# Kernel optimization log

Hardware: AMD Instinct MI355X
Metric: run time of the kernel (lower is better)

## Reference

```python
import jax, jax.numpy as jnp
import numpy as np

B, T, D = 1, 2048, 2048
H, KVH, G, HD = 32, 8, 4, 64  # n_heads, n_kv_heads, n_groups, head_dim


def _rope_angles(t, hd):
    # standard RoPE angle table: [T, hd//2]
    inv_freq = 1.0 / (10000.0 ** (jnp.arange(0, hd, 2, dtype=jnp.float32) / hd))
    return jnp.arange(t, dtype=jnp.float32)[:, None] * inv_freq[None, :]


def setup_inputs() -> dict:
    key = jax.random.key(0)
    k1, k2, k3, k4, k5 = jax.random.split(key, 5)
    scale = 0.02
    return {
        "x": jax.random.normal(k1, (B, T, D), dtype=jnp.float32),
        "freqs": _rope_angles(T, HD),                                  # [T, HD//2]
        "wq": jax.random.normal(k2, (D, H * HD), dtype=jnp.float32) * scale,
        "wk": jax.random.normal(k3, (D, KVH * HD), dtype=jnp.float32) * scale,
        "wv": jax.random.normal(k4, (D, KVH * HD), dtype=jnp.float32) * scale,
        "wo": jax.random.normal(k5, (H * HD, D), dtype=jnp.float32) * scale,
    }


def _apply_rope(t, cos, sin):
    # t: [B, T, nh, HD]; cos/sin: [T, HD//2] -> broadcast [1, T, 1, HD//2]
    t1, t2 = t[..., ::2], t[..., 1::2]
    c = cos[None, :, None, :]
    s = sin[None, :, None, :]
    out_even = t1 * c - t2 * s
    out_odd = t1 * s + t2 * c
    return jnp.stack([out_even, out_odd], axis=-1).reshape(t.shape)


def reference(x, freqs, wq, wk, wv, wo):
    b, t, _ = x.shape
    q = (x @ wq).reshape(b, t, H, HD)
    k = (x @ wk).reshape(b, t, KVH, HD)
    v = (x @ wv).reshape(b, t, KVH, HD)

    cos, sin = jnp.cos(freqs), jnp.sin(freqs)
    q = _apply_rope(q, cos, sin)
    k = _apply_rope(k, cos, sin)

    # GQA: repeat_interleave along head dim (kv head h -> query heads h*G..h*G+G-1)
    k = jnp.repeat(k, G, axis=2)  # [b, t, H, HD]
    v = jnp.repeat(v, G, axis=2)

    scale = 1.0 / jnp.sqrt(jnp.asarray(HD, dtype=x.dtype))
    scores = jnp.einsum("bthd,bshd->bhts", q, k) * scale  # [b, H, t, t]
    causal = jnp.tril(jnp.ones((t, t), dtype=bool))
    scores = jnp.where(causal[None, None], scores, jnp.asarray(-jnp.inf, dtype=scores.dtype))
    attn = jax.nn.softmax(scores, axis=-1)

    out = jnp.einsum("bhts,bshd->bthd", attn, v).reshape(b, t, H * HD)
    return out @ wo
```

## Files before the change

kernel.cpp:

```cpp
#include <hip/hip_runtime.h>
#include <cstdint>
#include <cstddef>

#define T_SEQ 2048
#define D_MODEL 2048
#define NH 32
#define NKVH 8
#define HDIM 64

typedef _Float16 f16;
typedef __attribute__((ext_vector_type(8))) _Float16 half8;
typedef __attribute__((ext_vector_type(4))) _Float16 half4;
typedef __attribute__((ext_vector_type(4))) float floatx4;

#define QSCALE 0.1803368801111204f

#if __has_builtin(__builtin_amdgcn_exp2f)
#define EXP2F(x) __builtin_amdgcn_exp2f(x)
#else
#define EXP2F(x) exp2f(x)
#endif


__device__ __forceinline__ void gload_lds16(const void* g, void* l) {
  __builtin_amdgcn_global_load_lds(
      (const __attribute__((address_space(1))) void*)g,
      (__attribute__((address_space(3))) void*)l,
      16, 0, 0);
}

__global__ __launch_bounds__(256) void cvt_f16_kernel(const float* __restrict__ in,
                                                      f16* __restrict__ out, int n4) {
  int id = blockIdx.x * 256 + threadIdx.x;
  if (id >= n4) return;
  int t = id >> 9;
  int d0 = (id & 511) * 4;
  float4 v = ((const float4*)in)[id];
  half4 o;
  o[0] = (f16)v.x; o[1] = (f16)v.y; o[2] = (f16)v.z; o[3] = (f16)v.w;
  int bm = t >> 7, mtb = (t & 127) >> 4, l15 = t & 15;
  int kt = d0 >> 6, s = (d0 & 63) >> 5, quad = (d0 & 31) >> 3, j = d0 & 7;
  size_t off = ((size_t)bm * 32 + kt) * 8192 + mtb * 1024 + s * 512 + (quad * 16 + l15) * 8 + j;
  *(half4*)&out[off] = o;
}

__global__ __launch_bounds__(256) void transpose_wqkv_kernel(const float* __restrict__ wq,
                                                             const float* __restrict__ wk,
                                                             const float* __restrict__ wv,
                                                             f16* __restrict__ out) {
  __shared__ f16 tile[64 * 65];
  int tid = threadIdx.x;
  int bx = blockIdx.x, kt = blockIdx.y;
  const float* in;
  int N, outN0, inCol0;
  if (bx < 32)      { in = wq; N = 2048; outN0 = 0;    inCol0 = bx * 64; }
  else if (bx < 40) { in = wk; N = 512;  outN0 = 2048; inCol0 = (bx - 32) * 64; }
  else              { in = wv; N = 512;  outN0 = 2560; inCol0 = (bx - 40) * 64; }
  int k0 = kt * 64;
#pragma unroll
  for (int i = 0; i < 16; i++) {
    int idx = i * 256 + tid;
    int kk = idx >> 6, nn = idx & 63;
    tile[nn * 65 + kk] = (f16)in[(size_t)(k0 + kk) * N + inCol0 + nn];
  }
  __syncthreads();
#pragma unroll
  for (int i = 0; i < 2; i++) {
    int idx = i * 256 + tid;
    int dd = idx >> 3, c = idx & 7;
    half8 v8 = *(const half8*)&tile[dd * 65 + c * 8];
    int ng = outN0 + inCol0 + dd;
    int bn = ng >> 7, ntb = (ng & 127) >> 4, l15 = ng & 15;
    int s = c >> 2, quad = c & 3;
    *(half8*)&out[((size_t)bn * 32 + kt) * 8192 + ntb * 1024 + s * 512 + (quad * 16 + l15) * 8] = v8;
  }
}

__global__ __launch_bounds__(256) void transpose_w_kernel(const float* __restrict__ in,
                                                          f16* __restrict__ out,
                                                          int N, int outN0) {
  __shared__ f16 tile[64 * 65];
  int tid = threadIdx.x;
  int inCol0 = blockIdx.x * 64, kt = blockIdx.y;
  int k0 = kt * 64;
#pragma unroll
  for (int i = 0; i < 16; i++) {
    int idx = i * 256 + tid;
    int kk = idx >> 6, nn = idx & 63;
    tile[nn * 65 + kk] = (f16)in[(size_t)(k0 + kk) * N + inCol0 + nn];
  }
  __syncthreads();
#pragma unroll
  for (int i = 0; i < 2; i++) {
    int idx = i * 256 + tid;
    int dd = idx >> 3, c = idx & 7;
    half8 v8 = *(const half8*)&tile[dd * 65 + c * 8];
    int ng = outN0 + inCol0 + dd;
    int bn = ng >> 7, ntb = (ng & 127) >> 4, l15 = ng & 15;
    int s = c >> 2, quad = c & 3;
    *(half8*)&out[((size_t)bn * 32 + kt) * 8192 + ntb * 1024 + s * 512 + (quad * 16 + l15) * 8] = v8;
  }
}

template <typename OutT>
__global__ __launch_bounds__(256) void gemm_f16_kernel(const f16* __restrict__ A,
                                                       const f16* __restrict__ BT,
                                                       OutT* __restrict__ C,
                                                       int M, int N, int K) {
  __shared__ alignas(16) f16 As[2][8192];
  __shared__ alignas(16) f16 Bs[2][8192];
  int tid = threadIdx.x;
  int wave = tid >> 6, lane = tid & 63;
  int ln15 = lane & 15, quad = lane >> 4;
  int wr = wave >> 1, wc = wave & 1;
  int bm = blockIdx.y, bn = blockIdx.x;
  int ktiles = K >> 6;
  const f16* Ab = A + (size_t)bm * ktiles * 8192;
  const f16* Bb = BT + (size_t)bn * ktiles * 8192;
  floatx4 acc[4][4];
  floatx4 zero = {0.f, 0.f, 0.f, 0.f};
#pragma unroll
  for (int mt = 0; mt < 4; mt++)
#pragma unroll
    for (int nt = 0; nt < 4; nt++) acc[mt][nt] = zero;

  auto stageg = [&](int kt, int buf) {
    const f16* at = Ab + (size_t)kt * 8192;
    const f16* bt = Bb + (size_t)kt * 8192;
#pragma unroll
    for (int i = 0; i < 4; i++) {
      gload_lds16(at + (wave * 4 + i) * 512 + lane * 8, &As[buf][(wave * 4 + i) * 512]);
      gload_lds16(bt + (wave * 4 + i) * 512 + lane * 8, &Bs[buf][(wave * 4 + i) * 512]);
    }
  };

  stageg(0, 0);
  for (int kt = 0; kt < ktiles; kt++) {
    int cur = kt & 1;
    if (kt + 1 < ktiles) {
      stageg(kt + 1, cur ^ 1);
      asm volatile("s_waitcnt vmcnt(8)\n\ts_barrier" ::: "memory");
    } else {
      asm volatile("s_waitcnt vmcnt(0)\n\ts_barrier" ::: "memory");
    }
#pragma unroll
    for (int s = 0; s < 2; s++) {
      half8 af[4], bf[4];
#pragma unroll
      for (int mt = 0; mt < 4; mt++)
        af[mt] = *(const half8*)&As[cur][(wr * 4 + mt) * 1024 + s * 512 + lane * 8];
#pragma unroll
      for (int nt = 0; nt < 4; nt++)
        bf[nt] = *(const half8*)&Bs[cur][(wc * 4 + nt) * 1024 + s * 512 + lane * 8];
#pragma unroll
      for (int mt = 0; mt < 4; mt++)
#pragma unroll
        for (int nt = 0; nt < 4; nt++)
          acc[mt][nt] = __builtin_amdgcn_mfma_f32_16x16x32_f16(af[mt], bf[nt], acc[mt][nt], 0, 0, 0);
    }
    if (kt + 1 < ktiles) {
      asm volatile("s_waitcnt lgkmcnt(0)\n\ts_barrier" ::: "memory");
    }
  }
  size_t rbase = (size_t)bm * 128 + wr * 64;
  int cbase = bn * 128 + wc * 64;
#pragma unroll
  for (int mt = 0; mt < 4; mt++)
#pragma unroll
    for (int nt = 0; nt < 4; nt++)
#pragma unroll
      for (int r = 0; r < 4; r++)
        C[(rbase + mt * 16 + quad * 4 + r) * (size_t)N + cbase + nt * 16 + ln15] =
            (OutT)acc[mt][nt][r];
}

__global__ __launch_bounds__(256) void rope_split_kernel(const f16* __restrict__ qkv,
                                                         const float* __restrict__ freqs,
                                                         f16* __restrict__ qr,
                                                         f16* __restrict__ katt) {
  int id = blockIdx.x * 256 + threadIdx.x;
  int t = id / 1280;
  int pr = id - t * 1280;
  int c0 = pr * 2;
  const f16* row = qkv + (size_t)t * 3072;
  if (c0 < 2048) {
    int h = c0 >> 6, p = (c0 & 63) >> 1;
    float ang = freqs[t * 32 + p];
    float s, c;
    __sincosf(ang, &s, &c);
    float t1 = (float)row[c0], t2 = (float)row[c0 + 1];
    f16* dst = qr + ((size_t)h * T_SEQ + t) * 64 + (c0 & 63);
    dst[0] = (f16)((t1 * c - t2 * s) * QSCALE);
    dst[1] = (f16)((t1 * s + t2 * c) * QSCALE);
  } else {
    int cc = c0 - 2048;
    int kh = cc >> 6, p = (cc & 63) >> 1;
    int d = cc & 63;
    float ang = freqs[t * 32 + p];
    float s, c;
    __sincosf(ang, &s, &c);
    float t1 = (float)row[2048 + cc], t2 = (float)row[2048 + cc + 1];
    int jt = t >> 6, nt = (t & 63) >> 4, ln15 = t & 15;
    int sfr = d >> 5, quad = (d & 31) >> 3, j = d & 7;
    f16* dst = katt + ((size_t)kh * 32 + jt) * 4096 + (nt * 2 + sfr) * 512 +
               (quad * 16 + ln15) * 8 + j;
    dst[0] = (f16)(t1 * c - t2 * s);
    dst[1] = (f16)(t1 * s + t2 * c);
  }
}

__global__ __launch_bounds__(256) void transpose_v_kernel(const f16* __restrict__ qkv,
                                                          f16* __restrict__ vatt) {
  __shared__ f16 tile[64 * 65];
  int tid = threadIdx.x;
  int head = blockIdx.y;
  int jt = blockIdx.x;
  int t0 = jt * 64;
#pragma unroll
  for (int i = 0; i < 16; i++) {
    int idx = i * 256 + tid;
    int tt = idx >> 6, dd = idx & 63;
    tile[dd * 65 + tt] = qkv[(size_t)(t0 + tt) * 3072 + 2560 + head * 64 + dd];
  }
  __syncthreads();
  f16* vtile = vatt + ((size_t)head * 32 + jt) * 4096;
#pragma unroll
  for (int i = 0; i < 2; i++) {
    int idx = i * 256 + tid;
    int dd = idx >> 3, c = idx & 7;
    half8 v8 = *(const half8*)&tile[dd * 65 + c * 8];
    int nt = dd >> 4, sfr = c >> 2, quad = c & 3, ln15 = dd & 15;
    *(half8*)&vtile[(nt * 2 + sfr) * 512 + (quad * 16 + ln15) * 8] = v8;
  }
}

__global__ __launch_bounds__(256) void attn_fwd_kernel(const f16* __restrict__ q,
                                                       const f16* __restrict__ katt,
                                                       const f16* __restrict__ vatt,
                                                       f16* __restrict__ ao) {
  __shared__ alignas(16) f16 Ks[3][4096];
  __shared__ alignas(16) f16 Vs[3][4096];
  __shared__ alignas(16) f16 Pq[4 * 1024];

  int tid = threadIdx.x;
  int lane = tid & 63, w = tid >> 6;
  int ln15 = lane & 15, quad = lane >> 4;
  int x = blockIdx.x;
  int h = blockIdx.y;
  int kvh = h >> 2;
  int qtA = x, qtB = 31 - x;
  int qbaseA = qtA * 64 + w * 16, qbaseB = qtB * 64 + w * 16;
  int qglobA = qbaseA + ln15, qglobB = qbaseB + ln15;

  const f16* kh = katt + (size_t)kvh * 32 * 4096;
  const f16* vh = vatt + (size_t)kvh * 32 * 4096;
  f16* P = &Pq[w * 1024];

  const f16* qhA = q + ((size_t)h * T_SEQ + qbaseA) * 64;
  const f16* qhB = q + ((size_t)h * T_SEQ + qbaseB) * 64;
  half8 qfA[2], qfB[2];
#pragma unroll
  for (int s = 0; s < 2; s++) {
    qfA[s] = *(const half8*)&qhA[(size_t)ln15 * 64 + s * 32 + quad * 8];
    qfB[s] = *(const half8*)&qhB[(size_t)ln15 * 64 + s * 32 + quad * 8];
  }

  floatx4 oaccA[4], oaccB[4];
  floatx4 zero = {0.f, 0.f, 0.f, 0.f};
#pragma unroll
  for (int nt = 0; nt < 4; nt++) { oaccA[nt] = zero; oaccB[nt] = zero; }
  float lA = 0.f, lB = 0.f;

  auto stage = [&](int jt, int buf) {
    const f16* kt = kh + (size_t)jt * 4096;
    const f16* vtile = vh + (size_t)jt * 4096;
    gload_lds16(kt + (w * 2 + 0) * 512 + lane * 8, &Ks[buf][(w * 2 + 0) * 512]);
    gload_lds16(kt + (w * 2 + 1) * 512 + lane * 8, &Ks[buf][(w * 2 + 1) * 512]);
    gload_lds16(vtile + (w * 2 + 0) * 512 + lane * 8, &Vs[buf][(w * 2 + 0) * 512]);
    gload_lds16(vtile + (w * 2 + 1) * 512 + lane * 8, &Vs[buf][(w * 2 + 1) * 512]);
  };

  auto compute_tile = [&](const half8* qf, floatx4* oacc, float& lsum, bool diag,
                          int qglob, int jt, int cur) {
    floatx4 sacc[4];
    __builtin_amdgcn_s_setprio(1);
#pragma unroll
    for (int nt = 0; nt < 4; nt++) {
      half8 kf0 = *(const half8*)&Ks[cur][(nt * 2 + 0) * 512 + lane * 8];
      half8 kf1 = *(const half8*)&Ks[cur][(nt * 2 + 1) * 512 + lane * 8];
      sacc[nt] = __builtin_amdgcn_mfma_f32_16x16x32_f16(kf0, qf[0], zero, 0, 0, 0);
      sacc[nt] = __builtin_amdgcn_mfma_f32_16x16x32_f16(kf1, qf[1], sacc[nt], 0, 0, 0);
    }
    __builtin_amdgcn_s_setprio(0);
    if (diag) {
#pragma unroll
      for (int nt = 0; nt < 4; nt++)
#pragma unroll
        for (int r = 0; r < 4; r++) {
          int keyg = jt * 64 + nt * 16 + quad * 4 + r;
          if (keyg > qglob) sacc[nt][r] = -1e30f;
        }
    }
    float sum = 0.f;
#pragma unroll
    for (int nt = 0; nt < 4; nt++) {
      float p0 = EXP2F(sacc[nt][0]);
      float p1 = EXP2F(sacc[nt][1]);
      float p2 = EXP2F(sacc[nt][2]);
      float p3 = EXP2F(sacc[nt][3]);
      sum += (p0 + p1) + (p2 + p3);
      half4 ph;
      ph[0] = (f16)p0; ph[1] = (f16)p1; ph[2] = (f16)p2; ph[3] = (f16)p3;
      *(half4*)&P[(nt >> 1) * 512 + (((nt & 1) * 2 + (quad >> 1)) * 16 + ln15) * 8 +
                  (quad & 1) * 4] = ph;
    }
    lsum += sum;
    asm volatile("s_waitcnt lgkmcnt(0)" ::: "memory");
    half8 pf0 = *(const half8*)&P[lane * 8];
    half8 pf1 = *(const half8*)&P[512 + lane * 8];
    __builtin_amdgcn_s_setprio(1);
#pragma unroll
    for (int nt = 0; nt < 4; nt++) {
      half8 vf0 = *(const half8*)&Vs[cur][(nt * 2 + 0) * 512 + lane * 8];
      half8 vf1 = *(const half8*)&Vs[cur][(nt * 2 + 1) * 512 + lane * 8];
      oacc[nt] = __builtin_amdgcn_mfma_f32_16x16x32_f16(vf0, pf0, oacc[nt], 0, 0, 0);
      oacc[nt] = __builtin_amdgcn_mfma_f32_16x16x32_f16(vf1, pf1, oacc[nt], 0, 0, 0);
    }
    __builtin_amdgcn_s_setprio(0);
  };

  int rounds = qtB + 1;
  stage(0, 0);
  stage(1, 1);
  asm volatile("s_waitcnt vmcnt(4) lgkmcnt(0)\n\ts_barrier" ::: "memory");
  for (int jt = 0; jt < rounds; jt++) {
    int cur = jt % 3;
    if (jt + 2 < rounds) stage(jt + 2, (jt + 2) % 3);
    if (jt <= qtA) compute_tile(qfA, oaccA, lA, jt == qtA, qglobA, jt, cur);
    compute_tile(qfB, oaccB, lB, jt == qtB, qglobB, jt, cur);
    if (jt + 2 < rounds) {
      asm volatile("s_waitcnt vmcnt(4) lgkmcnt(0)\n\ts_barrier" ::: "memory");
    } else if (jt + 1 < rounds) {
      asm volatile("s_waitcnt vmcnt(0) lgkmcnt(0)\n\ts_barrier" ::: "memory");
    }
  }

  lA += __shfl_xor(lA, 16);
  lA += __shfl_xor(lA, 32);
  lB += __shfl_xor(lB, 16);
  lB += __shfl_xor(lB, 32);

  float invA = 1.f / lA, invB = 1.f / lB;
  size_t abaseA = (((size_t)(qglobA >> 7)) * 32 + h) * 8192 + ((qbaseA & 127) >> 4) * 1024;
  size_t abaseB = (((size_t)(qglobB >> 7)) * 32 + h) * 8192 + ((qbaseB & 127) >> 4) * 1024;
#pragma unroll
  for (int nt = 0; nt < 4; nt++) {
    half4 ovA, ovB;
#pragma unroll
    for (int r = 0; r < 4; r++) {
      ovA[r] = (f16)(oaccA[nt][r] * invA);
      ovB[r] = (f16)(oaccB[nt][r] * invB);
    }
    int sA = nt >> 1;
    int quadA = (nt & 1) * 2 + (quad >> 1);
    int jA = (quad & 1) * 4;
    size_t foff = sA * 512 + (quadA * 16 + ln15) * 8 + jA;
    *(half4*)&ao[abaseA + foff] = ovA;
    *(half4*)&ao[abaseB + foff] = ovB;
  }
}

extern "C" void kernel_launch(void* const* d_in, const int* in_sizes, int n_in,
                              void* d_out, int out_size, void* d_ws, size_t ws_size,
                              hipStream_t stream) {
  (void)in_sizes; (void)n_in; (void)out_size;
  const float* x = (const float*)d_in[0];
  const float* freqs = (const float*)d_in[1];
  const float* wq = (const float*)d_in[2];
  const float* wk = (const float*)d_in[3];
  const float* wv = (const float*)d_in[4];
  const float* wo = (const float*)d_in[5];
  float* out = (float*)d_out;
  char* ws = (char*)d_ws;
  const size_t MB = 1024 * 1024;

  if (ws_size < 28 * MB) return;

  f16* xb = (f16*)(ws);
  f16* qr = (f16*)(ws);
  f16* wcatT = (f16*)(ws + 8 * MB);
  f16* katt = (f16*)(ws + 8 * MB);
  f16* vatt = (f16*)(ws + 10 * MB);
  f16* woT = (f16*)(ws + 12 * MB);
  f16* ao = (f16*)(ws + 20 * MB);
  f16* qkvh = (f16*)d_out;

  cvt_f16_kernel<<<(T_SEQ * D_MODEL / 4 + 255) / 256, 256, 0, stream>>>(x, xb, T_SEQ * D_MODEL / 4);
  transpose_wqkv_kernel<<<dim3(48, 32), 256, 0, stream>>>(wq, wk, wv, wcatT);
  gemm_f16_kernel<f16><<<dim3(3072 / 128, 2048 / 128), 256, 0, stream>>>(xb, wcatT, qkvh,
                                                                         2048, 3072, 2048);
  rope_split_kernel<<<(T_SEQ * 1280) / 256, 256, 0, stream>>>(qkvh, freqs, qr, katt);
  transpose_v_kernel<<<dim3(T_SEQ / 64, NKVH), 256, 0, stream>>>(qkvh, vatt);
  transpose_w_kernel<<<dim3(32, 32), 256, 0, stream>>>(wo, woT, 2048, 0);
  attn_fwd_kernel<<<dim3(16, NH), 256, 0, stream>>>(qr, katt, vatt, ao);
  gemm_f16_kernel<float><<<dim3(2048 / 128, 2048 / 128), 256, 0, stream>>>(ao, woT, out,
                                                                           2048, 2048, 2048);
}
```

Baseline: 243.8 us.

## Split attention KV loop across two wave groups with LDS combine

The attention block grows from 256 to 512 threads. Two groups of four waves each process alternating KV tiles for the same query rows, so each block's sequential KV loop is halved. At the end, partial accumulators and row sums are merged through shared memory before normalisation and the store. This raises parallelism for a grid of only 512 blocks, but it adds LDS usage (double-buffered per group), extra barriers per step, and a final combine.

```diff
diff --git a/kernel.cpp b/kernel.cpp
--- a/kernel.cpp
+++ b/kernel.cpp
@@ -234,22 +234,25 @@
   }
 }
 
-__global__ __launch_bounds__(256) void attn_fwd_kernel(const f16* __restrict__ q,
-                                                       const f16* __restrict__ katt,
-                                                       const f16* __restrict__ vatt,
-                                                       f16* __restrict__ ao) {
-  __shared__ alignas(16) f16 Ks[3][4096];
-  __shared__ alignas(16) f16 Vs[3][4096];
-  __shared__ alignas(16) f16 Pq[4 * 1024];
+__global__ __launch_bounds__(512, 4) void attn_fwd_kernel(const f16* __restrict__ q,
+                                                          const f16* __restrict__ katt,
+                                                          const f16* __restrict__ vatt,
+                                                          f16* __restrict__ ao) {
+  __shared__ alignas(16) f16 Ks[4][4096];
+  __shared__ alignas(16) f16 Vs[4][4096];
+  __shared__ alignas(16) f16 Pq[8 * 1024];
 
   int tid = threadIdx.x;
   int lane = tid & 63, w = tid >> 6;
+  int g = w >> 2, wl = w & 3;
   int ln15 = lane & 15, quad = lane >> 4;
   int x = blockIdx.x;
   int h = blockIdx.y;
   int kvh = h >> 2;
   int qtA = x, qtB = 31 - x;
-  int qbaseA = qtA * 64 + w * 16, qbaseB = qtB * 64 + w * 16;
+  int R = qtB + 1;
+  int S = (R + 1) >> 1;
+  int qbaseA = qtA * 64 + wl * 16, qbaseB = qtB * 64 + wl * 16;
   int qglobA = qbaseA + ln15, qglobB = qbaseB + ln15;
 
   const f16* kh = katt + (size_t)kvh * 32 * 4096;
@@ -271,23 +274,27 @@
   for (int nt = 0; nt < 4; nt++) { oaccA[nt] = zero; oaccB[nt] = zero; }
   float lA = 0.f, lB = 0.f;
 
-  auto stage = [&](int jt, int buf) {
-    const f16* kt = kh + (size_t)jt * 4096;
-    const f16* vtile = vh + (size_t)jt * 4096;
-    gload_lds16(kt + (w * 2 + 0) * 512 + lane * 8, &Ks[buf][(w * 2 + 0) * 512]);
-    gload_lds16(kt + (w * 2 + 1) * 512 + lane * 8, &Ks[buf][(w * 2 + 1) * 512]);
-    gload_lds16(vtile + (w * 2 + 0) * 512 + lane * 8, &Vs[buf][(w * 2 + 0) * 512]);
-    gload_lds16(vtile + (w * 2 + 1) * 512 + lane * 8, &Vs[buf][(w * 2 + 1) * 512]);
+  auto stage_pair = [&](int s1) {
+    int jtw = 2 * s1 + g;
+    if (jtw < R) {
+      int buf = ((s1 & 1) << 1) | g;
+      const f16* kt = kh + (size_t)jtw * 4096;
+      const f16* vt = vh + (size_t)jtw * 4096;
+      gload_lds16(kt + (wl * 2 + 0) * 512 + lane * 8, &Ks[buf][(wl * 2 + 0) * 512]);
+      gload_lds16(kt + (wl * 2 + 1) * 512 + lane * 8, &Ks[buf][(wl * 2 + 1) * 512]);
+      gload_lds16(vt + (wl * 2 + 0) * 512 + lane * 8, &Vs[buf][(wl * 2 + 0) * 512]);
+      gload_lds16(vt + (wl * 2 + 1) * 512 + lane * 8, &Vs[buf][(wl * 2 + 1) * 512]);
+    }
   };
 
   auto compute_tile = [&](const half8* qf, floatx4* oacc, float& lsum, bool diag,
-                          int qglob, int jt, int cur) {
+                          int qglob, int jt, int buf) {
     floatx4 sacc[4];
     __builtin_amdgcn_s_setprio(1);
 #pragma unroll
     for (int nt = 0; nt < 4; nt++) {
-      half8 kf0 = *(const half8*)&Ks[cur][(nt * 2 + 0) * 512 + lane * 8];
-      half8 kf1 = *(const half8*)&Ks[cur][(nt * 2 + 1) * 512 + lane * 8];
+      half8 kf0 = *(const half8*)&Ks[buf][(nt * 2 + 0) * 512 + lane * 8];
+      half8 kf1 = *(const half8*)&Ks[buf][(nt * 2 + 1) * 512 + lane * 8];
       sacc[nt] = __builtin_amdgcn_mfma_f32_16x16x32_f16(kf0, qf[0], zero, 0, 0, 0);
       sacc[nt] = __builtin_amdgcn_mfma_f32_16x16x32_f16(kf1, qf[1], sacc[nt], 0, 0, 0);
     }
@@ -321,52 +328,78 @@
     __builtin_amdgcn_s_setprio(1);
 #pragma unroll
     for (int nt = 0; nt < 4; nt++) {
-      half8 vf0 = *(const half8*)&Vs[cur][(nt * 2 + 0) * 512 + lane * 8];
-      half8 vf1 = *(const half8*)&Vs[cur][(nt * 2 + 1) * 512 + lane * 8];
+      half8 vf0 = *(const half8*)&Vs[buf][(nt * 2 + 0) * 512 + lane * 8];
+      half8 vf1 = *(const half8*)&Vs[buf][(nt * 2 + 1) * 512 + lane * 8];
       oacc[nt] = __builtin_amdgcn_mfma_f32_16x16x32_f16(vf0, pf0, oacc[nt], 0, 0, 0);
       oacc[nt] = __builtin_amdgcn_mfma_f32_16x16x32_f16(vf1, pf1, oacc[nt], 0, 0, 0);
     }
     __builtin_amdgcn_s_setprio(0);
   };
 
-  int rounds = qtB + 1;
-  stage(0, 0);
-  stage(1, 1);
-  asm volatile("s_waitcnt vmcnt(4) lgkmcnt(0)\n\ts_barrier" ::: "memory");
-  for (int jt = 0; jt < rounds; jt++) {
-    int cur = jt % 3;
-    if (jt + 2 < rounds) stage(jt + 2, (jt + 2) % 3);
-    if (jt <= qtA) compute_tile(qfA, oaccA, lA, jt == qtA, qglobA, jt, cur);
-    compute_tile(qfB, oaccB, lB, jt == qtB, qglobB, jt, cur);
-    if (jt + 2 < rounds) {
-      asm volatile("s_waitcnt vmcnt(4) lgkmcnt(0)\n\ts_barrier" ::: "memory");
-    } else if (jt + 1 < rounds) {
+  stage_pair(0);
+  for (int s = 0; s < S; s++) {
+    int jt = 2 * s + g;
+    int buf = ((s & 1) << 1) | g;
+    if (s + 1 < S) {
+      stage_pair(s + 1);
+      if (2 * (s + 1) + g < R)
+        asm volatile("s_waitcnt vmcnt(4) lgkmcnt(0)\n\ts_barrier" ::: "memory");
+      else
+        asm volatile("s_waitcnt vmcnt(0) lgkmcnt(0)\n\ts_barrier" ::: "memory");
+    } else {
       asm volatile("s_waitcnt vmcnt(0) lgkmcnt(0)\n\ts_barrier" ::: "memory");
     }
-  }
-
-  lA += __shfl_xor(lA, 16);
-  lA += __shfl_xor(lA, 32);
-  lB += __shfl_xor(lB, 16);
-  lB += __shfl_xor(lB, 32);
-
-  float invA = 1.f / lA, invB = 1.f / lB;
-  size_t abaseA = (((size_t)(qglobA >> 7)) * 32 + h) * 8192 + ((qbaseA & 127) >> 4) * 1024;
-  size_t abaseB = (((size_t)(qglobB >> 7)) * 32 + h) * 8192 + ((qbaseB & 127) >> 4) * 1024;
-#pragma unroll
-  for (int nt = 0; nt < 4; nt++) {
-    half4 ovA, ovB;
-#pragma unroll
-    for (int r = 0; r < 4; r++) {
-      ovA[r] = (f16)(oaccA[nt][r] * invA);
-      ovB[r] = (f16)(oaccB[nt][r] * invB);
-    }
-    int sA = nt >> 1;
-    int quadA = (nt & 1) * 2 + (quad >> 1);
-    int jA = (quad & 1) * 4;
-    size_t foff = sA * 512 + (quadA * 16 + ln15) * 8 + jA;
-    *(half4*)&ao[abaseA + foff] = ovA;
-    *(half4*)&ao[abaseB + foff] = ovB;
+    if (jt < R) {
+      if (jt <= qtA) compute_tile(qfA, oaccA, lA, jt == qtA, qglobA, jt, buf);
+      compute_tile(qfB, oaccB, lB, jt == qtB, qglobB, jt, buf);
+    }
+    if (s + 1 < S)
+      asm volatile("s_waitcnt lgkmcnt(0)\n\ts_barrier" ::: "memory");
+  }
+
+  floatx4* comb4 = (floatx4*)&Ks[0][0];
+  float* combf = (float*)&Ks[0][0];
+  int cslot = (wl * 64 + lane) * 10;
+  asm volatile("s_waitcnt lgkmcnt(0)\n\ts_barrier" ::: "memory");
+  if (g == 1) {
+#pragma unroll
+    for (int nt = 0; nt < 4; nt++) comb4[cslot + nt] = oaccA[nt];
+#pragma unroll
+    for (int nt = 0; nt < 4; nt++) comb4[cslot + 4 + nt] = oaccB[nt];
+    combf[(cslot + 8) * 4 + 0] = lA;
+    combf[(cslot + 8) * 4 + 1] = lB;
+  }
+  asm volatile("s_waitcnt lgkmcnt(0)\n\ts_barrier" ::: "memory");
+  if (g == 0) {
+#pragma unroll
+    for (int nt = 0; nt < 4; nt++) {
+      oaccA[nt] += comb4[cslot + nt];
+      oaccB[nt] += comb4[cslot + 4 + nt];
+    }
+    lA += combf[(cslot + 8) * 4 + 0];
+    lB += combf[(cslot + 8) * 4 + 1];
+    lA += __shfl_xor(lA, 16);
+    lA += __shfl_xor(lA, 32);
+    lB += __shfl_xor(lB, 16);
+    lB += __shfl_xor(lB, 32);
+    float invA = 1.f / lA, invB = 1.f / lB;
+    size_t abaseA = (((size_t)(qglobA >> 7)) * 32 + h) * 8192 + ((qbaseA & 127) >> 4) * 1024;
+    size_t abaseB = (((size_t)(qglobB >> 7)) * 32 + h) * 8192 + ((qbaseB & 127) >> 4) * 1024;
+#pragma unroll
+    for (int nt = 0; nt < 4; nt++) {
+      half4 ovA, ovB;
+#pragma unroll
+      for (int r = 0; r < 4; r++) {
+        ovA[r] = (f16)(oaccA[nt][r] * invA);
+        ovB[r] = (f16)(oaccB[nt][r] * invB);
+      }
+      int sA = nt >> 1;
+      int quadA = (nt & 1) * 2 + (quad >> 1);
+      int jA = (quad & 1) * 4;
+      size_t foff = sA * 512 + (quadA * 16 + ln15) * 8 + jA;
+      *(half4*)&ao[abaseA + foff] = ovA;
+      *(half4*)&ao[abaseB + foff] = ovB;
+    }
   }
 }
 
@@ -402,7 +435,7 @@
   rope_split_kernel<<<(T_SEQ * 1280) / 256, 256, 0, stream>>>(qkvh, freqs, qr, katt);
   transpose_v_kernel<<<dim3(T_SEQ / 64, NKVH), 256, 0, stream>>>(qkvh, vatt);
   transpose_w_kernel<<<dim3(32, 32), 256, 0, stream>>>(wo, woT, 2048, 0);
-  attn_fwd_kernel<<<dim3(16, NH), 256, 0, stream>>>(qr, katt, vatt, ao);
+  attn_fwd_kernel<<<dim3(16, NH), 512, 0, stream>>>(qr, katt, vatt, ao);
   gemm_f16_kernel<float><<<dim3(2048 / 128, 2048 / 128), 256, 0, stream>>>(ao, woT, out,
                                                                            2048, 2048, 2048);
 }
```

Measured after the change: 230.3 us. 1.06x faster.
